# Kernel optimization log

Measured on AMD Instinct MI355X. Metric: run time of the kernel, lower is better.

The kernel has to match this reference:

```python
import jax, jax.numpy as jnp
import numpy as np

N, E, IN, H, D = 20000, 640000, 256, 4, 32
NEG_SLOPE = 0.2


def setup_inputs() -> dict:
    key = jax.random.key(0)
    ks = jax.random.split(key, 8)
    feat = jax.random.normal(ks[0], (N, IN), dtype=jnp.float32)
    pr_score = jax.random.uniform(ks[1], (N,), dtype=jnp.float32) + 1e-3
    edge_src = jax.random.randint(ks[2], (E,), 0, N)
    edge_dst = jax.random.randint(ks[3], (E,), 0, N)
    # parameters (xavier-ish scale)
    fc_w = jax.random.normal(ks[4], (H * D, IN), dtype=jnp.float32) * (2.0 / np.sqrt(IN + H * D))
    attn_l = jax.random.normal(ks[5], (1, H, D), dtype=jnp.float32) * (2.0 / np.sqrt(1 + D))
    attn_r = jax.random.normal(ks[6], (1, H, D), dtype=jnp.float32) * (2.0 / np.sqrt(1 + D))
    bias = jnp.zeros((H * D,), dtype=jnp.float32)
    return {"feat": feat, "pr_score": pr_score, "edge_src": edge_src,
            "edge_dst": edge_dst, "fc_w": fc_w, "attn_l": attn_l,
            "attn_r": attn_r, "bias": bias}


def reference(feat, pr_score, edge_src, edge_dst, fc_w, attn_l, attn_r, bias):
    n = feat.shape[0]
    h, d = attn_l.shape[1], attn_l.shape[2]
    # feat_src = fc(feat).view(N, H, D)
    ft = (feat @ fc_w.T).reshape(n, h, d)                       # [N,H,D]
    el = jnp.sum(ft * attn_l, axis=-1)                          # [N,H]
    er = jnp.sum(ft * attn_r, axis=-1)                          # [N,H]
    e = jax.nn.leaky_relu(el[edge_src] + er[edge_dst], NEG_SLOPE)  # [E,H]
    # edge_softmax over incoming edges per destination node
    emax = jax.ops.segment_max(e, edge_dst, num_segments=n)
    ee = jnp.exp(e - emax[edge_dst])
    esum = jax.ops.segment_sum(ee, edge_dst, num_segments=n)
    a = ee / esum[edge_dst]                                     # [E,H]
    # PageRank-style normalization: b = pr[src] / sum_{in-edges}(pr[src])
    pr_src = pr_score[edge_src]                                 # [E]
    pr_sum = jax.ops.segment_sum(pr_src, edge_dst, num_segments=n)
    b = pr_src / pr_sum[edge_dst]                               # [E]
    c = a * b[:, None]                                          # [E,H]
    csum = jax.ops.segment_sum(c, edge_dst, num_segments=n)
    c = c / csum[edge_dst]                                      # [E,H]
    # weighted aggregation: rst[dst] = sum_e ft[src_e] * c_e
    m = ft[edge_src] * c[:, :, None]                            # [E,H,D]
    rst = jax.ops.segment_sum(m, edge_dst, num_segments=n)      # [N,H,D]
    rst = rst + bias.reshape(1, h, d)
    return rst
```

## Files before the change

### kernel.cpp

```cpp
#include <hip/hip_runtime.h>

#define IN_DIM 256
#define HD 128
#define NHEAD 4
#define NEG_SLOPE 0.2f
#define ELLW 128

typedef unsigned int  uint;
typedef unsigned short ushort_t;

typedef short bf16x8 __attribute__((ext_vector_type(8)));
typedef float f32x4  __attribute__((ext_vector_type(4)));

__device__ __forceinline__ ushort_t f2bf(float x) {
    uint u = __float_as_uint(x);
    u += 0x7fffu + ((u >> 16) & 1u);
    return (ushort_t)(u >> 16);
}
__device__ __forceinline__ uint pack2(float lo, float hi) {
    return (uint)f2bf(lo) | ((uint)f2bf(hi) << 16);
}
__device__ __forceinline__ float bflo(uint u) { return __uint_as_float(u << 16); }
__device__ __forceinline__ float bfhi(uint u) { return __uint_as_float(u & 0xffff0000u); }

#define GBM 64
#define GBK 64
#define LDK 72

__global__ __launch_bounds__(256) void gemm_mfma(
    const float* __restrict__ feat, const float* __restrict__ fcw,
    const float* __restrict__ attn_l, const float* __restrict__ attn_r,
    ushort_t* __restrict__ ft16, float* __restrict__ el, float* __restrict__ er,
    int* __restrict__ deg, int n)
{
    __shared__ ushort_t s_a[GBM * LDK];
    __shared__ ushort_t s_b[128 * LDK];

    const int t    = threadIdx.x;
    {
        const int z = blockIdx.x * 256 + t;
        if (z < n) deg[z] = 0;
    }

    const int row0 = blockIdx.x * GBM;
    const int w    = t >> 6;
    const int lane = t & 63;
    const int fr   = lane & 15;
    const int fq   = lane >> 4;

    f32x4 acc[8];
#pragma unroll
    for (int nt = 0; nt < 8; ++nt) acc[nt] = (f32x4){0.f, 0.f, 0.f, 0.f};

    const int s_row = t >> 2, s_kca = (t & 3) * 16;
    const int s_col = t >> 1, s_kcb = (t & 1) * 32;

    const ushort_t* pa  = &s_a[(w * 16 + fr) * LDK + fq * 8];
    const ushort_t* pb0 = &s_b[fr * LDK + fq * 8];

    for (int k0 = 0; k0 < IN_DIM; k0 += GBK) {
        {
            const int grow = row0 + s_row;
            float4 v0, v1, v2, v3;
            if (grow < n) {
                const float* p = feat + (size_t)grow * IN_DIM + k0 + s_kca;
                v0 = *(const float4*)(p + 0);
                v1 = *(const float4*)(p + 4);
                v2 = *(const float4*)(p + 8);
                v3 = *(const float4*)(p + 12);
            } else {
                v0 = make_float4(0.f,0.f,0.f,0.f); v1 = v0; v2 = v0; v3 = v0;
            }
            uint4* dst = (uint4*)&s_a[s_row * LDK + s_kca];
            dst[0] = make_uint4(pack2(v0.x,v0.y), pack2(v0.z,v0.w),
                                pack2(v1.x,v1.y), pack2(v1.z,v1.w));
            dst[1] = make_uint4(pack2(v2.x,v2.y), pack2(v2.z,v2.w),
                                pack2(v3.x,v3.y), pack2(v3.z,v3.w));
        }
        {
            const float* p = fcw + (size_t)s_col * IN_DIM + k0 + s_kcb;
            uint4* dst = (uint4*)&s_b[s_col * LDK + s_kcb];
#pragma unroll
            for (int q = 0; q < 2; ++q) {
                float4 u0 = *(const float4*)(p + q * 16 + 0);
                float4 u1 = *(const float4*)(p + q * 16 + 4);
                float4 u2 = *(const float4*)(p + q * 16 + 8);
                float4 u3 = *(const float4*)(p + q * 16 + 12);
                dst[2 * q + 0] = make_uint4(pack2(u0.x,u0.y), pack2(u0.z,u0.w),
                                            pack2(u1.x,u1.y), pack2(u1.z,u1.w));
                dst[2 * q + 1] = make_uint4(pack2(u2.x,u2.y), pack2(u2.z,u2.w),
                                            pack2(u3.x,u3.y), pack2(u3.z,u3.w));
            }
        }
        __syncthreads();

        const bf16x8 a0 = *(const bf16x8*)pa;
        const bf16x8 a1 = *(const bf16x8*)(pa + 32);
#pragma unroll
        for (int nt = 0; nt < 8; ++nt) {
            const ushort_t* pb = pb0 + nt * 16 * LDK;
            const bf16x8 b0 = *(const bf16x8*)pb;
            const bf16x8 b1 = *(const bf16x8*)(pb + 32);
            acc[nt] = __builtin_amdgcn_mfma_f32_16x16x32_bf16(a0, b0, acc[nt], 0, 0, 0);
            acc[nt] = __builtin_amdgcn_mfma_f32_16x16x32_bf16(a1, b1, acc[nt], 0, 0, 0);
        }
        __syncthreads();
    }

    float al[8], ar_[8];
#pragma unroll
    for (int nt = 0; nt < 8; ++nt) {
        al[nt]  = attn_l[nt * 16 + fr];
        ar_[nt] = attn_r[nt * 16 + fr];
    }

#pragma unroll
    for (int j = 0; j < 4; ++j) {
        const int grow = row0 + w * 16 + fq * 4 + j;
        const bool ok = grow < n;
        if (ok) {
#pragma unroll
            for (int nt = 0; nt < 8; ++nt)
                ft16[(size_t)grow * HD + nt * 16 + fr] = f2bf(acc[nt][j]);
        }
        float pl0 = acc[0][j]*al[0] + acc[1][j]*al[1];
        float pl1 = acc[2][j]*al[2] + acc[3][j]*al[3];
        float pl2 = acc[4][j]*al[4] + acc[5][j]*al[5];
        float pl3 = acc[6][j]*al[6] + acc[7][j]*al[7];
        float pe0 = acc[0][j]*ar_[0] + acc[1][j]*ar_[1];
        float pe1 = acc[2][j]*ar_[2] + acc[3][j]*ar_[3];
        float pe2 = acc[4][j]*ar_[4] + acc[5][j]*ar_[5];
        float pe3 = acc[6][j]*ar_[6] + acc[7][j]*ar_[7];
#pragma unroll
        for (int m = 1; m < 16; m <<= 1) {
            pl0 += __shfl_xor(pl0, m, 64); pl1 += __shfl_xor(pl1, m, 64);
            pl2 += __shfl_xor(pl2, m, 64); pl3 += __shfl_xor(pl3, m, 64);
            pe0 += __shfl_xor(pe0, m, 64); pe1 += __shfl_xor(pe1, m, 64);
            pe2 += __shfl_xor(pe2, m, 64); pe3 += __shfl_xor(pe3, m, 64);
        }
        if (ok && fr == 0) {
            *(float4*)&el[(size_t)grow * NHEAD] = make_float4(pl0, pl1, pl2, pl3);
            *(float4*)&er[(size_t)grow * NHEAD] = make_float4(pe0, pe1, pe2, pe3);
        }
    }
}

__global__ void build_ell(const int* __restrict__ src, const int* __restrict__ dst,
                          int* __restrict__ deg, int* __restrict__ ell, int e)
{
    int i = blockIdx.x * blockDim.x + threadIdx.x;
    if (i < e) {
        const int d = dst[i];
        const int r = atomicAdd(&deg[d], 1);
        if (r < ELLW) ell[(size_t)d * ELLW + r] = src[i];
    }
}

__global__ __launch_bounds__(256) void aggregate(
    const uint4* __restrict__ ftu4, const float* __restrict__ el,
    const float* __restrict__ er, const float* __restrict__ pr,
    const int* __restrict__ deg, const int* __restrict__ ell,
    const float* __restrict__ bias, float* __restrict__ out, int n)
{
    const int wave = threadIdx.x >> 6;
    const int lane = threadIdx.x & 63;
    const int slot = lane >> 4;
    const int sub  = lane & 15;
    const int head = sub >> 2;
    const int dst  = blockIdx.x * 4 + wave;

    __shared__ float s_w[4][NHEAD][72];
    __shared__ int   s_s[4][72];

    if (dst >= n) return;

    if (lane < 8) {
        s_s[wave][64 + lane] = 0;
#pragma unroll
        for (int hh = 0; hh < NHEAD; ++hh) s_w[wave][hh][64 + lane] = 0.f;
    }

    const int dg  = min(deg[dst], ELLW);
    const int beg = dst * ELLW;
    const float4 e4 = *(const float4*)&er[(size_t)dst * NHEAD];

    float aA[8], aB[8];
#pragma unroll
    for (int i = 0; i < 8; ++i) { aA[i] = 0.f; aB[i] = 0.f; }
    float wS = 0.f;

    for (int base = 0; base < dg; base += 64) {
        const int len = min(64, dg - base);
        if (lane < len) {
            const int s = ell[beg + base + lane];
            const float p = pr[s];
            const float4 l4 = *(const float4*)&el[(size_t)s * NHEAD];
            float e0 = l4.x + e4.x, e1 = l4.y + e4.y;
            float e2 = l4.z + e4.z, e3 = l4.w + e4.w;
            e0 = e0 > 0.f ? e0 : NEG_SLOPE * e0;
            e1 = e1 > 0.f ? e1 : NEG_SLOPE * e1;
            e2 = e2 > 0.f ? e2 : NEG_SLOPE * e2;
            e3 = e3 > 0.f ? e3 : NEG_SLOPE * e3;
            s_w[wave][0][lane] = __expf(e0) * p;
            s_w[wave][1][lane] = __expf(e1) * p;
            s_w[wave][2][lane] = __expf(e2) * p;
            s_w[wave][3][lane] = __expf(e3) * p;
            s_s[wave][lane] = s;
        } else {
            s_w[wave][0][lane] = 0.f; s_w[wave][1][lane] = 0.f;
            s_w[wave][2][lane] = 0.f; s_w[wave][3][lane] = 0.f;
            s_s[wave][lane] = 0;
        }
        for (int j = 0; j < len; j += 8) {
            const int eA = j + slot;
            const int eB = j + 4 + slot;
            const int   sA = s_s[wave][eA];
            const int   sB = s_s[wave][eB];
            const float wA = s_w[wave][head][eA];
            const float wB = s_w[wave][head][eB];
            const uint4 uA = ftu4[(size_t)sA * 16 + sub];
            const uint4 uB = ftu4[(size_t)sB * 16 + sub];
            wS += wA + wB;
            aA[0] = fmaf(wA, bflo(uA.x), aA[0]);
            aA[1] = fmaf(wA, bfhi(uA.x), aA[1]);
            aA[2] = fmaf(wA, bflo(uA.y), aA[2]);
            aA[3] = fmaf(wA, bfhi(uA.y), aA[3]);
            aA[4] = fmaf(wA, bflo(uA.z), aA[4]);
            aA[5] = fmaf(wA, bfhi(uA.z), aA[5]);
            aA[6] = fmaf(wA, bflo(uA.w), aA[6]);
            aA[7] = fmaf(wA, bfhi(uA.w), aA[7]);
            aB[0] = fmaf(wB, bflo(uB.x), aB[0]);
            aB[1] = fmaf(wB, bfhi(uB.x), aB[1]);
            aB[2] = fmaf(wB, bflo(uB.y), aB[2]);
            aB[3] = fmaf(wB, bfhi(uB.y), aB[3]);
            aB[4] = fmaf(wB, bflo(uB.z), aB[4]);
            aB[5] = fmaf(wB, bfhi(uB.z), aB[5]);
            aB[6] = fmaf(wB, bflo(uB.w), aB[6]);
            aB[7] = fmaf(wB, bfhi(uB.w), aB[7]);
        }
    }

    float a[8];
#pragma unroll
    for (int i = 0; i < 8; ++i) a[i] = aA[i] + aB[i];
#pragma unroll
    for (int i = 0; i < 8; ++i) {
        a[i] += __shfl_xor(a[i], 16, 64);
        a[i] += __shfl_xor(a[i], 32, 64);
    }
    wS += __shfl_xor(wS, 16, 64);
    wS += __shfl_xor(wS, 32, 64);

    if (slot == 0) {
        const float inv = (dg > 0) ? 1.f / wS : 0.f;
        const float4 b0 = *(const float4*)&bias[8 * sub];
        const float4 b1 = *(const float4*)&bias[8 * sub + 4];
        float4 r0, r1;
        r0.x = a[0] * inv + b0.x; r0.y = a[1] * inv + b0.y;
        r0.z = a[2] * inv + b0.z; r0.w = a[3] * inv + b0.w;
        r1.x = a[4] * inv + b1.x; r1.y = a[5] * inv + b1.y;
        r1.z = a[6] * inv + b1.z; r1.w = a[7] * inv + b1.w;
        *(float4*)&out[(size_t)dst * HD + 8 * sub]     = r0;
        *(float4*)&out[(size_t)dst * HD + 8 * sub + 4] = r1;
    }
}

extern "C" void kernel_launch(void* const* d_in, const int* in_sizes, int n_in,
                              void* d_out, int out_size, void* d_ws, size_t ws_size,
                              hipStream_t stream)
{
    const float* feat   = (const float*)d_in[0];
    const float* pr     = (const float*)d_in[1];
    const int*   esrc   = (const int*)d_in[2];
    const int*   edst   = (const int*)d_in[3];
    const float* fcw    = (const float*)d_in[4];
    const float* attn_l = (const float*)d_in[5];
    const float* attn_r = (const float*)d_in[6];
    const float* bias   = (const float*)d_in[7];
    float* out = (float*)d_out;

    const int n = in_sizes[0] / IN_DIM;
    const int e = in_sizes[2];

    char* ws = (char*)d_ws;
    size_t off = 0;
    auto wsalloc = [&](size_t bytes) -> void* {
        void* p = ws + off;
        off += (bytes + 255) & ~(size_t)255;
        return p;
    };
    ushort_t* ft16 = (ushort_t*)wsalloc((size_t)n * HD * sizeof(ushort_t));
    float* el   = (float*)wsalloc((size_t)n * NHEAD * sizeof(float));
    float* er   = (float*)wsalloc((size_t)n * NHEAD * sizeof(float));
    int*   deg  = (int*)wsalloc((size_t)n * sizeof(int));
    int*   ell  = (int*)wsalloc((size_t)n * ELLW * sizeof(int));

    gemm_mfma<<<(n + GBM - 1) / GBM, 256, 0, stream>>>(feat, fcw, attn_l, attn_r,
                                                       ft16, el, er, deg, n);
    build_ell<<<(e + 255) / 256, 256, 0, stream>>>(esrc, edst, deg, ell, e);
    aggregate<<<(n + 3) / 4, 256, 0, stream>>>((const uint4*)ft16, el, er, pr,
                                               deg, ell, bias, out, n);
}
```

Baseline: 80.47 us.

## Split GEMM columns across two blocks and pack pr score with el

The GEMM grid is doubled so each block computes 64 of the 128 output columns (two heads), which doubles the block count for better occupancy and halves per-block registers and LDS. el is widened to an 8-float record per node that also holds pr, so the aggregate gather fetches el and pr from one 32-byte line instead of two separate random loads. The cost is that each feat tile is now read and converted twice, and the el record is larger.

```diff
diff --git a/kernel.cpp b/kernel.cpp
--- a/kernel.cpp
+++ b/kernel.cpp
@@ -30,30 +30,34 @@
 __global__ __launch_bounds__(256) void gemm_mfma(
     const float* __restrict__ feat, const float* __restrict__ fcw,
     const float* __restrict__ attn_l, const float* __restrict__ attn_r,
-    ushort_t* __restrict__ ft16, float* __restrict__ el, float* __restrict__ er,
+    const float* __restrict__ pr,
+    ushort_t* __restrict__ ft16, float* __restrict__ elp, float* __restrict__ er,
     int* __restrict__ deg, int n)
 {
     __shared__ ushort_t s_a[GBM * LDK];
-    __shared__ ushort_t s_b[128 * LDK];
-
-    const int t    = threadIdx.x;
+    __shared__ ushort_t s_b[64 * LDK];
+
+    const int t = threadIdx.x;
     {
         const int z = blockIdx.x * 256 + t;
         if (z < n) deg[z] = 0;
     }
 
-    const int row0 = blockIdx.x * GBM;
+    const int tile = blockIdx.x >> 1;
+    const int half = blockIdx.x & 1;
+    const int row0 = tile * GBM;
+    const int col0 = half * 64;
     const int w    = t >> 6;
     const int lane = t & 63;
     const int fr   = lane & 15;
     const int fq   = lane >> 4;
 
-    f32x4 acc[8];
-#pragma unroll
-    for (int nt = 0; nt < 8; ++nt) acc[nt] = (f32x4){0.f, 0.f, 0.f, 0.f};
+    f32x4 acc[4];
+#pragma unroll
+    for (int nt = 0; nt < 4; ++nt) acc[nt] = (f32x4){0.f, 0.f, 0.f, 0.f};
 
     const int s_row = t >> 2, s_kca = (t & 3) * 16;
-    const int s_col = t >> 1, s_kcb = (t & 1) * 32;
+    const int s_col = t >> 2, s_kcb = (t & 3) * 16;
 
     const ushort_t* pa  = &s_a[(w * 16 + fr) * LDK + fq * 8];
     const ushort_t* pb0 = &s_b[fr * LDK + fq * 8];
@@ -78,26 +82,23 @@
                                 pack2(v3.x,v3.y), pack2(v3.z,v3.w));
         }
         {
-            const float* p = fcw + (size_t)s_col * IN_DIM + k0 + s_kcb;
+            const float* p = fcw + (size_t)(col0 + s_col) * IN_DIM + k0 + s_kcb;
+            float4 u0 = *(const float4*)(p + 0);
+            float4 u1 = *(const float4*)(p + 4);
+            float4 u2 = *(const float4*)(p + 8);
+            float4 u3 = *(const float4*)(p + 12);
             uint4* dst = (uint4*)&s_b[s_col * LDK + s_kcb];
-#pragma unroll
-            for (int q = 0; q < 2; ++q) {
-                float4 u0 = *(const float4*)(p + q * 16 + 0);
-                float4 u1 = *(const float4*)(p + q * 16 + 4);
-                float4 u2 = *(const float4*)(p + q * 16 + 8);
-                float4 u3 = *(const float4*)(p + q * 16 + 12);
-                dst[2 * q + 0] = make_uint4(pack2(u0.x,u0.y), pack2(u0.z,u0.w),
-                                            pack2(u1.x,u1.y), pack2(u1.z,u1.w));
-                dst[2 * q + 1] = make_uint4(pack2(u2.x,u2.y), pack2(u2.z,u2.w),
-                                            pack2(u3.x,u3.y), pack2(u3.z,u3.w));
-            }
+            dst[0] = make_uint4(pack2(u0.x,u0.y), pack2(u0.z,u0.w),
+                                pack2(u1.x,u1.y), pack2(u1.z,u1.w));
+            dst[1] = make_uint4(pack2(u2.x,u2.y), pack2(u2.z,u2.w),
+                                pack2(u3.x,u3.y), pack2(u3.z,u3.w));
         }
         __syncthreads();
 
         const bf16x8 a0 = *(const bf16x8*)pa;
         const bf16x8 a1 = *(const bf16x8*)(pa + 32);
 #pragma unroll
-        for (int nt = 0; nt < 8; ++nt) {
+        for (int nt = 0; nt < 4; ++nt) {
             const ushort_t* pb = pb0 + nt * 16 * LDK;
             const bf16x8 b0 = *(const bf16x8*)pb;
             const bf16x8 b1 = *(const bf16x8*)(pb + 32);
@@ -107,11 +108,12 @@
         __syncthreads();
     }
 
-    float al[8], ar_[8];
-#pragma unroll
-    for (int nt = 0; nt < 8; ++nt) {
-        al[nt]  = attn_l[nt * 16 + fr];
-        ar_[nt] = attn_r[nt * 16 + fr];
+    const int h0 = 2 * half;
+    float al[4], ar_[4];
+#pragma unroll
+    for (int nt = 0; nt < 4; ++nt) {
+        al[nt]  = attn_l[col0 + nt * 16 + fr];
+        ar_[nt] = attn_r[col0 + nt * 16 + fr];
     }
 
 #pragma unroll
@@ -120,27 +122,22 @@
         const bool ok = grow < n;
         if (ok) {
 #pragma unroll
-            for (int nt = 0; nt < 8; ++nt)
-                ft16[(size_t)grow * HD + nt * 16 + fr] = f2bf(acc[nt][j]);
-        }
-        float pl0 = acc[0][j]*al[0] + acc[1][j]*al[1];
-        float pl1 = acc[2][j]*al[2] + acc[3][j]*al[3];
-        float pl2 = acc[4][j]*al[4] + acc[5][j]*al[5];
-        float pl3 = acc[6][j]*al[6] + acc[7][j]*al[7];
-        float pe0 = acc[0][j]*ar_[0] + acc[1][j]*ar_[1];
-        float pe1 = acc[2][j]*ar_[2] + acc[3][j]*ar_[3];
-        float pe2 = acc[4][j]*ar_[4] + acc[5][j]*ar_[5];
-        float pe3 = acc[6][j]*ar_[6] + acc[7][j]*ar_[7];
+            for (int nt = 0; nt < 4; ++nt)
+                ft16[(size_t)grow * HD + col0 + nt * 16 + fr] = f2bf(acc[nt][j]);
+        }
+        float plA = acc[0][j]*al[0] + acc[1][j]*al[1];
+        float plB = acc[2][j]*al[2] + acc[3][j]*al[3];
+        float peA = acc[0][j]*ar_[0] + acc[1][j]*ar_[1];
+        float peB = acc[2][j]*ar_[2] + acc[3][j]*ar_[3];
 #pragma unroll
         for (int m = 1; m < 16; m <<= 1) {
-            pl0 += __shfl_xor(pl0, m, 64); pl1 += __shfl_xor(pl1, m, 64);
-            pl2 += __shfl_xor(pl2, m, 64); pl3 += __shfl_xor(pl3, m, 64);
-            pe0 += __shfl_xor(pe0, m, 64); pe1 += __shfl_xor(pe1, m, 64);
-            pe2 += __shfl_xor(pe2, m, 64); pe3 += __shfl_xor(pe3, m, 64);
+            plA += __shfl_xor(plA, m, 64); plB += __shfl_xor(plB, m, 64);
+            peA += __shfl_xor(peA, m, 64); peB += __shfl_xor(peB, m, 64);
         }
         if (ok && fr == 0) {
-            *(float4*)&el[(size_t)grow * NHEAD] = make_float4(pl0, pl1, pl2, pl3);
-            *(float4*)&er[(size_t)grow * NHEAD] = make_float4(pe0, pe1, pe2, pe3);
+            *(float2*)&elp[(size_t)grow * 8 + h0] = make_float2(plA, plB);
+            *(float2*)&er[(size_t)grow * NHEAD + h0] = make_float2(peA, peB);
+            if (half == 0) elp[(size_t)grow * 8 + 4] = pr[grow];
         }
     }
 }
@@ -157,8 +154,8 @@
 }
 
 __global__ __launch_bounds__(256) void aggregate(
-    const uint4* __restrict__ ftu4, const float* __restrict__ el,
-    const float* __restrict__ er, const float* __restrict__ pr,
+    const uint4* __restrict__ ftu4, const float* __restrict__ elp,
+    const float* __restrict__ er,
     const int* __restrict__ deg, const int* __restrict__ ell,
     const float* __restrict__ bias, float* __restrict__ out, int n)
 {
@@ -193,8 +190,8 @@
         const int len = min(64, dg - base);
         if (lane < len) {
             const int s = ell[beg + base + lane];
-            const float p = pr[s];
-            const float4 l4 = *(const float4*)&el[(size_t)s * NHEAD];
+            const float4 l4 = *(const float4*)&elp[(size_t)s * 8];
+            const float p   = elp[(size_t)s * 8 + 4];
             float e0 = l4.x + e4.x, e1 = l4.y + e4.y;
             float e2 = l4.z + e4.z, e3 = l4.w + e4.w;
             e0 = e0 > 0.f ? e0 : NEG_SLOPE * e0;
@@ -290,14 +287,15 @@
         return p;
     };
     ushort_t* ft16 = (ushort_t*)wsalloc((size_t)n * HD * sizeof(ushort_t));
-    float* el   = (float*)wsalloc((size_t)n * NHEAD * sizeof(float));
+    float* elp  = (float*)wsalloc((size_t)n * 8 * sizeof(float));
     float* er   = (float*)wsalloc((size_t)n * NHEAD * sizeof(float));
     int*   deg  = (int*)wsalloc((size_t)n * sizeof(int));
     int*   ell  = (int*)wsalloc((size_t)n * ELLW * sizeof(int));
 
-    gemm_mfma<<<(n + GBM - 1) / GBM, 256, 0, stream>>>(feat, fcw, attn_l, attn_r,
-                                                       ft16, el, er, deg, n);
+    const int ntiles = (n + GBM - 1) / GBM;
+    gemm_mfma<<<2 * ntiles, 256, 0, stream>>>(feat, fcw, attn_l, attn_r, pr,
+                                              ft16, elp, er, deg, n);
     build_ell<<<(e + 255) / 256, 256, 0, stream>>>(esrc, edst, deg, ell, e);
-    aggregate<<<(n + 3) / 4, 256, 0, stream>>>((const uint4*)ft16, el, er, pr,
+    aggregate<<<(n + 3) / 4, 256, 0, stream>>>((const uint4*)ft16, elp, er,
                                                deg, ell, bias, out, n);
 }
```

New measurement: 74.36 us. 7.6% less time.
